# Kernel optimization log

Measured on AMD Instinct MI355X. Metric: run time of the kernel, lower is better.

Reference implementation:

```python
import jax, jax.numpy as jnp
import numpy as np

B, T, D, H, C = 128, 256, 512, 1024, 1000
FORGET_BIAS = 1.0  # tf BasicLSTMCell default


def setup_inputs() -> dict:
    key = jax.random.key(0)
    k0, k1, k2, k3 = jax.random.split(key, 4)
    x = jax.random.normal(k0, (B, T, D), dtype=jnp.float32)
    # BasicLSTMCell kernel: [D+H, 4H] (gate order i, j, f, o); bias zero-init in TF
    Wk = jax.random.normal(k1, (D + H, 4 * H), dtype=jnp.float32) * 0.01
    bk = jnp.zeros((4 * H,), dtype=jnp.float32)
    # Output projection (truncated_normal(0, 0.01) in source; plain normal ok for reference)
    w = jax.random.normal(k2, (H, C), dtype=jnp.float32) * 0.01
    b = jax.random.normal(k3, (C,), dtype=jnp.float32) * 0.01
    return {"x": x, "Wk": Wk, "bk": bk, "w": w, "b": b}


def reference(x, Wk, bk, w, b):
    Bq, Tq, Dq = x.shape
    Hq = w.shape[0]

    def step(carry, xt):
        h, c = carry
        z = jnp.concatenate([xt, h], axis=-1) @ Wk + bk  # [B, 4H]
        i, j, f, o = jnp.split(z, 4, axis=-1)            # gate order i, j, f, o
        c_new = c * jax.nn.sigmoid(f + FORGET_BIAS) + jax.nn.sigmoid(i) * jnp.tanh(j)
        h_new = jax.nn.sigmoid(o) * jnp.tanh(c_new)
        return (h_new, c_new), None

    h0 = jnp.zeros((Bq, Hq), dtype=x.dtype)
    c0 = jnp.zeros((Bq, Hq), dtype=x.dtype)
    (hT, _), _ = jax.lax.scan(step, (h0, c0), jnp.swapaxes(x, 0, 1))  # scan over T
    return hT @ w + b  # [B, C]
```

## Files before the change

### kernel.cpp

```cpp
#include <hip/hip_runtime.h>
#include <math.h>

#define B 128
#define T 256
#define D 512
#define H 1024
#define KTOT 1536
#define N4 4096

#define HSTRIDE ((size_t)B * H + 2048)

typedef short short8 __attribute__((ext_vector_type(8)));
typedef float f32x16 __attribute__((ext_vector_type(16)));

__device__ __forceinline__ unsigned short f2bf(float f) {
    unsigned int u = __builtin_bit_cast(unsigned int, f);
    unsigned int r = (u + 0x7fffu + ((u >> 16) & 1u)) >> 16;
    return (unsigned short)r;
}
__device__ __forceinline__ float bf2f(unsigned short s) {
    unsigned int u = ((unsigned int)s) << 16;
    return __builtin_bit_cast(float, u);
}
__device__ __forceinline__ float sigm(float x) { return 1.f / (1.f + __expf(-x)); }
__device__ __forceinline__ float tanh_fast(float x) {
    return 1.f - 2.f / (1.f + __expf(2.f * x));
}

__global__ __launch_bounds__(256) void convert_x(
    const float* __restrict__ x, unsigned short* __restrict__ xb)
{
    int bid = blockIdx.x;
    int t = bid >> 7;
    int b = bid & 127;
    int d = threadIdx.x * 2;
    const float2 v = *(const float2*)&x[((size_t)b * T + t) * D + d];
    unsigned int packed = (unsigned int)f2bf(v.x) | ((unsigned int)f2bf(v.y) << 16);
    *(unsigned int*)&xb[((size_t)t * B + b) * D + d] = packed;
}

__global__ __launch_bounds__(256) void convert_W(
    const float* __restrict__ Wk, unsigned short* __restrict__ Wp)
{
    __shared__ float tile[32][33];
    int nb = blockIdx.x;
    int kb = blockIdx.y;
    int tx = threadIdx.x & 31;
    int ty = threadIdx.x >> 5;
    #pragma unroll
    for (int i = 0; i < 4; ++i) {
        int k = kb * 32 + ty + i * 8;
        tile[ty + i * 8][tx] = Wk[(size_t)k * N4 + nb * 32 + tx];
    }
    __syncthreads();
    #pragma unroll
    for (int i = 0; i < 4; ++i) {
        int n = nb * 32 + ty + i * 8;
        int pcol = ((n & 1023) << 2) | (n >> 10);
        Wp[(size_t)pcol * KTOT + kb * 32 + tx] = f2bf(tile[tx][ty + i * 8]);
    }
}

__global__ __launch_bounds__(256, 1) void lstm_persist(
    const unsigned short* __restrict__ xb,
    const unsigned short* __restrict__ Wp,
    const float* __restrict__ bk,
    unsigned short* __restrict__ hring,
    unsigned int* __restrict__ arr)
{
    __shared__ float zbuf[4][64][36];
    __shared__ unsigned short hbuf[32][20];

    const int tid  = threadIdx.x;
    const int bi   = blockIdx.x;
    const int rg   = (bi & 7) >> 1;
    const int cg   = ((bi >> 3) << 1) | (bi & 1);
    const int kq   = tid >> 6;
    const int lane = tid & 63;
    const int l31  = lane & 31;
    const int lhi  = lane >> 5;

    const int row = rg * 32 + l31;

    short8 wb[48];
    const unsigned short* wb0 = Wp + (size_t)(cg * 64 + l31) * KTOT + lhi * 8;
    const unsigned short* wb1 = wb0 + (size_t)32 * KTOT;
    #pragma unroll
    for (int j = 0; j < 8; ++j) {
        int k = (kq * 8 + j) * 16;
        wb[2 * j]     = *(const short8*)(wb0 + k);
        wb[2 * j + 1] = *(const short8*)(wb1 + k);
    }
    #pragma unroll
    for (int j = 0; j < 16; ++j) {
        int k = 512 + (kq * 16 + j) * 16;
        wb[16 + 2 * j]     = *(const short8*)(wb0 + k);
        wb[16 + 2 * j + 1] = *(const short8*)(wb1 + k);
    }

    float bi_[2], bj_[2], bf_[2], bo_[2];
    #pragma unroll
    for (int u = 0; u < 2; ++u) {
        int e   = tid + u * 256;
        int hcl = e >> 5;
        int hcg = cg * 16 + hcl;
        bi_[u] = bk[hcg];
        bj_[u] = bk[H + hcg];
        bf_[u] = bk[2 * H + hcg] + 1.0f;
        bo_[u] = bk[3 * H + hcg];
    }
    float cs0 = 0.f, cs1 = 0.f;

    const unsigned int* const fpoll = arr + rg * 256 + kq * 64 + lane;
    unsigned int* const fmine = arr + rg * 256 + cg * 4 + kq;
    const unsigned short* const xbase = xb + (size_t)row * D + kq * 128 + lhi * 8;
    const size_t hoff = (size_t)(rg * 64 + kq * 16) * 512 + l31 * 16 + lhi * 8;
    const size_t soff = (size_t)(rg * 64 + cg) * 256;

    const f32x16 fz = {0.f,0.f,0.f,0.f,0.f,0.f,0.f,0.f,
                       0.f,0.f,0.f,0.f,0.f,0.f,0.f,0.f};

    for (int t = 0; t < T; ++t) {
        f32x16 a00 = fz, a01 = fz, a10 = fz, a11 = fz;

        const unsigned short* xr = xbase + (size_t)t * (B * D);
        short8 xv[8];
        #pragma unroll
        for (int j = 0; j < 8; ++j)
            xv[j] = *(const short8*)(xr + j * 16);

        if (t > 0) {
            unsigned fv = __hip_atomic_load(fpoll, __ATOMIC_RELAXED,
                                            __HIP_MEMORY_SCOPE_AGENT);
            unsigned long long rb = __ballot(fv >= (unsigned)t);
            const unsigned short* hp = hring + (size_t)(t - 1) * HSTRIDE + hoff;
            short8 hv[16];
            #pragma unroll
            for (int j = 0; j < 16; ++j) {
                while (((rb >> (4 * j)) & 0xFull) != 0xFull) {
                    fv = __hip_atomic_load(fpoll, __ATOMIC_RELAXED,
                                           __HIP_MEMORY_SCOPE_AGENT);
                    rb = __ballot(fv >= (unsigned)t);
                }
                asm volatile("" ::: "memory");
                hv[j] = *(const short8*)(hp + j * 512);
                if (j < 8) {
                    if (j & 1) {
                        a10 = __builtin_amdgcn_mfma_f32_32x32x16_bf16(xv[j], wb[2 * j],     a10, 0, 0, 0);
                        a11 = __builtin_amdgcn_mfma_f32_32x32x16_bf16(xv[j], wb[2 * j + 1], a11, 0, 0, 0);
                    } else {
                        a00 = __builtin_amdgcn_mfma_f32_32x32x16_bf16(xv[j], wb[2 * j],     a00, 0, 0, 0);
                        a01 = __builtin_amdgcn_mfma_f32_32x32x16_bf16(xv[j], wb[2 * j + 1], a01, 0, 0, 0);
                    }
                }
            }
            #pragma unroll
            for (int j = 0; j < 16; ++j) {
                if (j & 1) {
                    a10 = __builtin_amdgcn_mfma_f32_32x32x16_bf16(hv[j], wb[16 + 2 * j],     a10, 0, 0, 0);
                    a11 = __builtin_amdgcn_mfma_f32_32x32x16_bf16(hv[j], wb[16 + 2 * j + 1], a11, 0, 0, 0);
                } else {
                    a00 = __builtin_amdgcn_mfma_f32_32x32x16_bf16(hv[j], wb[16 + 2 * j],     a00, 0, 0, 0);
                    a01 = __builtin_amdgcn_mfma_f32_32x32x16_bf16(hv[j], wb[16 + 2 * j + 1], a01, 0, 0, 0);
                }
            }
        } else {
            #pragma unroll
            for (int j = 0; j < 8; ++j) {
                if (j & 1) {
                    a10 = __builtin_amdgcn_mfma_f32_32x32x16_bf16(xv[j], wb[2 * j],     a10, 0, 0, 0);
                    a11 = __builtin_amdgcn_mfma_f32_32x32x16_bf16(xv[j], wb[2 * j + 1], a11, 0, 0, 0);
                } else {
                    a00 = __builtin_amdgcn_mfma_f32_32x32x16_bf16(xv[j], wb[2 * j],     a00, 0, 0, 0);
                    a01 = __builtin_amdgcn_mfma_f32_32x32x16_bf16(xv[j], wb[2 * j + 1], a01, 0, 0, 0);
                }
            }
        }

        f32x16 z0 = a00 + a10;
        f32x16 z1 = a01 + a11;

        #pragma unroll
        for (int q = 0; q < 4; ++q) {
            float4 v0 = { z0[4 * q + 0], z0[4 * q + 1], z0[4 * q + 2], z0[4 * q + 3] };
            *(float4*)&zbuf[kq][l31][lhi * 4 + q * 8] = v0;
            float4 v1 = { z1[4 * q + 0], z1[4 * q + 1], z1[4 * q + 2], z1[4 * q + 3] };
            *(float4*)&zbuf[kq][32 + l31][lhi * 4 + q * 8] = v1;
        }
        __syncthreads();

        #pragma unroll
        for (int u = 0; u < 2; ++u) {
            int e   = tid + u * 256;
            int r   = e & 31;
            int hcl = e >> 5;
            int pcb = hcl * 4;
            float zi = zbuf[0][pcb + 0][r] + zbuf[1][pcb + 0][r]
                     + zbuf[2][pcb + 0][r] + zbuf[3][pcb + 0][r] + bi_[u];
            float zj = zbuf[0][pcb + 1][r] + zbuf[1][pcb + 1][r]
                     + zbuf[2][pcb + 1][r] + zbuf[3][pcb + 1][r] + bj_[u];
            float zf = zbuf[0][pcb + 2][r] + zbuf[1][pcb + 2][r]
                     + zbuf[2][pcb + 2][r] + zbuf[3][pcb + 2][r] + bf_[u];
            float zo = zbuf[0][pcb + 3][r] + zbuf[1][pcb + 3][r]
                     + zbuf[2][pcb + 3][r] + zbuf[3][pcb + 3][r] + bo_[u];
            float& cc = u ? cs1 : cs0;
            float cn = cc * sigm(zf) + sigm(zi) * tanh_fast(zj);
            cc = cn;
            float hn = sigm(zo) * tanh_fast(cn);
            hbuf[r][hcl] = f2bf(hn);
        }
        __syncthreads();

        {
            int r  = tid >> 3;
            int cp = tid & 7;
            unsigned int v = *(const unsigned int*)&hbuf[r][cp * 2];
            unsigned int* hdst = (unsigned int*)(hring + (size_t)t * HSTRIDE);
            __hip_atomic_store(&hdst[soff + tid], v,
                               __ATOMIC_RELAXED, __HIP_MEMORY_SCOPE_AGENT);
        }
        if (t != T - 1) {
            asm volatile("s_waitcnt vmcnt(0)" ::: "memory");
            if (lane == 0)
                __hip_atomic_store(fmine, (unsigned)(t + 1),
                                   __ATOMIC_RELAXED, __HIP_MEMORY_SCOPE_AGENT);
        }
    }
}

__global__ __launch_bounds__(256) void proj_kernel(
    const unsigned short* __restrict__ hb, const float* __restrict__ w,
    const float* __restrict__ bias, float* __restrict__ out)
{
    int cidx = blockIdx.x * 256 + threadIdx.x;
    int bg   = blockIdx.y;
    bool valid = cidx < 1000;
    float acc[16];
    #pragma unroll
    for (int i = 0; i < 16; ++i) acc[i] = 0.f;

    for (int k = 0; k < H; k += 4) {
        float w0 = 0.f, w1 = 0.f, w2 = 0.f, w3 = 0.f;
        if (valid) {
            w0 = w[(size_t)(k + 0) * 1000 + cidx];
            w1 = w[(size_t)(k + 1) * 1000 + cidx];
            w2 = w[(size_t)(k + 2) * 1000 + cidx];
            w3 = w[(size_t)(k + 3) * 1000 + cidx];
        }
        #pragma unroll
        for (int i = 0; i < 16; ++i) {
            int row = bg * 16 + i;
            size_t a = (size_t)((row >> 5) * 64 + (k >> 4)) * 512
                     + (size_t)(row & 31) * 16 + (k & 15);
            ushort4 hv = *(const ushort4*)&hb[a];
            acc[i] += bf2f(hv.x) * w0 + bf2f(hv.y) * w1
                    + bf2f(hv.z) * w2 + bf2f(hv.w) * w3;
        }
    }
    if (valid) {
        #pragma unroll
        for (int i = 0; i < 16; ++i)
            out[(size_t)(bg * 16 + i) * 1000 + cidx] = acc[i] + bias[cidx];
    }
}

extern "C" void kernel_launch(void* const* d_in, const int* in_sizes, int n_in,
                              void* d_out, int out_size, void* d_ws, size_t ws_size,
                              hipStream_t stream) {
    const float* x  = (const float*)d_in[0];
    const float* Wk = (const float*)d_in[1];
    const float* bk = (const float*)d_in[2];
    const float* w  = (const float*)d_in[3];
    const float* b  = (const float*)d_in[4];
    float* out = (float*)d_out;

    char* p = (char*)d_ws;
    unsigned short* xb = (unsigned short*)p;  p += (size_t)B * T * D * 2;
    unsigned short* Wp = (unsigned short*)p;  p += (size_t)N4 * KTOT * 2;
    unsigned short* hr = (unsigned short*)p;  p += HSTRIDE * T * 2;
    unsigned int*   ar = (unsigned int*)p;    p += 4 * 64 * 4 * 4;

    hipMemsetAsync(ar, 0, 4 * 64 * 4 * 4, stream);

    convert_x<<<dim3(T * B), dim3(256), 0, stream>>>(x, xb);
    convert_W<<<dim3(N4 / 32, KTOT / 32), dim3(256), 0, stream>>>(Wk, Wp);

    lstm_persist<<<dim3(256), dim3(256), 0, stream>>>(xb, Wp, bk, hr, ar);

    proj_kernel<<<dim3(4, 8), dim3(256), 0, stream>>>(hr + (size_t)(T - 1) * HSTRIDE,
                                                      w, b, out);
}
```

Measured before the change: 1.324 ms.

## Remap gate threads to drop hbuf barrier, double-buffer zbuf, hoist x-MFMAs before poll

Each thread now computes the two adjacent hidden columns for one batch row that it later stores, so the h values are packed straight from registers. This removes the hbuf shared array and one __syncthreads per timestep. zbuf is double-buffered by timestep parity with padding changed to 37, so the next step's writes cannot race the previous step's reads without a second barrier. The input-projection MFMAs are issued before the flag wait so they run under the poll latency, and the flag load is issued earlier. The scalar LDS stores replace float4 stores, which may add LDS instructions.

After: 2.035 ms. 53.7% more time.

```diff
diff --git a/kernel.cpp b/kernel.cpp
--- a/kernel.cpp
+++ b/kernel.cpp
@@ -68,8 +68,7 @@
     unsigned short* __restrict__ hring,
     unsigned int* __restrict__ arr)
 {
-    __shared__ float zbuf[4][64][36];
-    __shared__ unsigned short hbuf[32][20];
+    __shared__ float zbuf[2][4][64][37];
 
     const int tid  = threadIdx.x;
     const int bi   = blockIdx.x;
@@ -98,12 +97,12 @@
         wb[16 + 2 * j + 1] = *(const short8*)(wb1 + k);
     }
 
+    const int gr2 = 8 * kq + (lane >> 3);
+    const int cp2 = lane & 7;
     float bi_[2], bj_[2], bf_[2], bo_[2];
     #pragma unroll
     for (int u = 0; u < 2; ++u) {
-        int e   = tid + u * 256;
-        int hcl = e >> 5;
-        int hcg = cg * 16 + hcl;
+        int hcg = cg * 16 + cp2 * 2 + u;
         bi_[u] = bk[hcg];
         bj_[u] = bk[H + hcg];
         bf_[u] = bk[2 * H + hcg] + 1.0f;
@@ -123,36 +122,40 @@
     for (int t = 0; t < T; ++t) {
         f32x16 a00 = fz, a01 = fz, a10 = fz, a11 = fz;
 
+        unsigned fv = 0;
+        if (t > 0)
+            fv = __hip_atomic_load(fpoll, __ATOMIC_RELAXED,
+                                   __HIP_MEMORY_SCOPE_AGENT);
+
         const unsigned short* xr = xbase + (size_t)t * (B * D);
         short8 xv[8];
         #pragma unroll
         for (int j = 0; j < 8; ++j)
             xv[j] = *(const short8*)(xr + j * 16);
+        #pragma unroll
+        for (int j = 0; j < 8; ++j) {
+            if (j & 1) {
+                a10 = __builtin_amdgcn_mfma_f32_32x32x16_bf16(xv[j], wb[2 * j],     a10, 0, 0, 0);
+                a11 = __builtin_amdgcn_mfma_f32_32x32x16_bf16(xv[j], wb[2 * j + 1], a11, 0, 0, 0);
+            } else {
+                a00 = __builtin_amdgcn_mfma_f32_32x32x16_bf16(xv[j], wb[2 * j],     a00, 0, 0, 0);
+                a01 = __builtin_amdgcn_mfma_f32_32x32x16_bf16(xv[j], wb[2 * j + 1], a01, 0, 0, 0);
+            }
+        }
 
         if (t > 0) {
-            unsigned fv = __hip_atomic_load(fpoll, __ATOMIC_RELAXED,
-                                            __HIP_MEMORY_SCOPE_AGENT);
             unsigned long long rb = __ballot(fv >= (unsigned)t);
             const unsigned short* hp = hring + (size_t)(t - 1) * HSTRIDE + hoff;
             short8 hv[16];
             #pragma unroll
             for (int j = 0; j < 16; ++j) {
                 while (((rb >> (4 * j)) & 0xFull) != 0xFull) {
-                    fv = __hip_atomic_load(fpoll, __ATOMIC_RELAXED,
-                                           __HIP_MEMORY_SCOPE_AGENT);
-                    rb = __ballot(fv >= (unsigned)t);
+                    unsigned f2 = __hip_atomic_load(fpoll, __ATOMIC_RELAXED,
+                                                    __HIP_MEMORY_SCOPE_AGENT);
+                    rb = __ballot(f2 >= (unsigned)t);
                 }
                 asm volatile("" ::: "memory");
                 hv[j] = *(const short8*)(hp + j * 512);
-                if (j < 8) {
-                    if (j & 1) {
-                        a10 = __builtin_amdgcn_mfma_f32_32x32x16_bf16(xv[j], wb[2 * j],     a10, 0, 0, 0);
-                        a11 = __builtin_amdgcn_mfma_f32_32x32x16_bf16(xv[j], wb[2 * j + 1], a11, 0, 0, 0);
-                    } else {
-                        a00 = __builtin_amdgcn_mfma_f32_32x32x16_bf16(xv[j], wb[2 * j],     a00, 0, 0, 0);
-                        a01 = __builtin_amdgcn_mfma_f32_32x32x16_bf16(xv[j], wb[2 * j + 1], a01, 0, 0, 0);
-                    }
-                }
             }
             #pragma unroll
             for (int j = 0; j < 16; ++j) {
@@ -164,57 +167,43 @@
                     a01 = __builtin_amdgcn_mfma_f32_32x32x16_bf16(hv[j], wb[16 + 2 * j + 1], a01, 0, 0, 0);
                 }
             }
-        } else {
-            #pragma unroll
-            for (int j = 0; j < 8; ++j) {
-                if (j & 1) {
-                    a10 = __builtin_amdgcn_mfma_f32_32x32x16_bf16(xv[j], wb[2 * j],     a10, 0, 0, 0);
-                    a11 = __builtin_amdgcn_mfma_f32_32x32x16_bf16(xv[j], wb[2 * j + 1], a11, 0, 0, 0);
-                } else {
-                    a00 = __builtin_amdgcn_mfma_f32_32x32x16_bf16(xv[j], wb[2 * j],     a00, 0, 0, 0);
-                    a01 = __builtin_amdgcn_mfma_f32_32x32x16_bf16(xv[j], wb[2 * j + 1], a01, 0, 0, 0);
-                }
-            }
         }
 
         f32x16 z0 = a00 + a10;
         f32x16 z1 = a01 + a11;
 
+        float (*zb)[64][37] = zbuf[t & 1];
         #pragma unroll
         for (int q = 0; q < 4; ++q) {
-            float4 v0 = { z0[4 * q + 0], z0[4 * q + 1], z0[4 * q + 2], z0[4 * q + 3] };
-            *(float4*)&zbuf[kq][l31][lhi * 4 + q * 8] = v0;
-            float4 v1 = { z1[4 * q + 0], z1[4 * q + 1], z1[4 * q + 2], z1[4 * q + 3] };
-            *(float4*)&zbuf[kq][32 + l31][lhi * 4 + q * 8] = v1;
+            #pragma unroll
+            for (int i = 0; i < 4; ++i) {
+                int r = i + 8 * q + 4 * lhi;
+                zb[kq][l31][r]      = z0[4 * q + i];
+                zb[kq][32 + l31][r] = z1[4 * q + i];
+            }
         }
         __syncthreads();
 
+        unsigned short hbf[2];
         #pragma unroll
         for (int u = 0; u < 2; ++u) {
-            int e   = tid + u * 256;
-            int r   = e & 31;
-            int hcl = e >> 5;
-            int pcb = hcl * 4;
-            float zi = zbuf[0][pcb + 0][r] + zbuf[1][pcb + 0][r]
-                     + zbuf[2][pcb + 0][r] + zbuf[3][pcb + 0][r] + bi_[u];
-            float zj = zbuf[0][pcb + 1][r] + zbuf[1][pcb + 1][r]
-                     + zbuf[2][pcb + 1][r] + zbuf[3][pcb + 1][r] + bj_[u];
-            float zf = zbuf[0][pcb + 2][r] + zbuf[1][pcb + 2][r]
-                     + zbuf[2][pcb + 2][r] + zbuf[3][pcb + 2][r] + bf_[u];
-            float zo = zbuf[0][pcb + 3][r] + zbuf[1][pcb + 3][r]
-                     + zbuf[2][pcb + 3][r] + zbuf[3][pcb + 3][r] + bo_[u];
+            int pcb = (cp2 * 2 + u) * 4;
+            float zi = zb[0][pcb + 0][gr2] + zb[1][pcb + 0][gr2]
+                     + zb[2][pcb + 0][gr2] + zb[3][pcb + 0][gr2] + bi_[u];
+            float zj = zb[0][pcb + 1][gr2] + zb[1][pcb + 1][gr2]
+                     + zb[2][pcb + 1][gr2] + zb[3][pcb + 1][gr2] + bj_[u];
+            float zf = zb[0][pcb + 2][gr2] + zb[1][pcb + 2][gr2]
+                     + zb[2][pcb + 2][gr2] + zb[3][pcb + 2][gr2] + bf_[u];
+            float zo = zb[0][pcb + 3][gr2] + zb[1][pcb + 3][gr2]
+                     + zb[2][pcb + 3][gr2] + zb[3][pcb + 3][gr2] + bo_[u];
             float& cc = u ? cs1 : cs0;
             float cn = cc * sigm(zf) + sigm(zi) * tanh_fast(zj);
             cc = cn;
-            float hn = sigm(zo) * tanh_fast(cn);
-            hbuf[r][hcl] = f2bf(hn);
-        }
-        __syncthreads();
+            hbf[u] = f2bf(sigm(zo) * tanh_fast(cn));
+        }
 
         {
-            int r  = tid >> 3;
-            int cp = tid & 7;
-            unsigned int v = *(const unsigned int*)&hbuf[r][cp * 2];
+            unsigned int v = (unsigned int)hbf[0] | ((unsigned int)hbf[1] << 16);
             unsigned int* hdst = (unsigned int*)(hring + (size_t)t * HSTRIDE);
             __hip_atomic_store(&hdst[soff + tid], v,
                                __ATOMIC_RELAXED, __HIP_MEMORY_SCOPE_AGENT);
```
